# Performance work log

Hardware: AMD Instinct MI355X
Metric: run time of the kernel (lower is better)

The kernel has to match this reference:

```python
import jax, jax.numpy as jnp
import numpy as np

NX, NY = 512, 512
NT = 240
STRIDE = 4
H = 1e-3
DT = 5e-8
F0 = 100000.0
T0 = 6e-6
AMP = 1.0
GAUSS_A = 5e6
RHO = 1600.0
C_INIT = dict(C11=1e11, C22=1e10, C12=8e9, C16=2.5e10, C26=3e9, C66=1.2e10)
C_LO, C_HI = 1e9, 1e13


def setup_inputs() -> dict:
    # Ricker wavelet source signal (full time resolution)
    t = np.arange(NT) * DT
    tau = t - T0
    pf = (np.pi * F0 * tau) ** 2
    signal = (AMP * (1.0 - 2.0 * pf) * np.exp(-pf)).astype(np.float32)
    # Gaussian point-load spatial distribution centered at (0,0)
    Lx, Ly = H * (NX - 1), H * (NY - 1)
    x = np.linspace(-Lx / 2, Lx / 2, NX, dtype=np.float64)
    y = np.linspace(-Ly / 2, Ly / 2, NY, dtype=np.float64)
    X, Y = np.meshgrid(x, y, indexing='ij')
    r2 = X ** 2 + Y ** 2
    gauss = (GAUSS_A / np.pi * np.exp(-GAUSS_A * r2)).astype(np.float32)
    return {
        'log_C11': jnp.array([np.log(C_INIT['C11'])], dtype=jnp.float32),
        'log_C22': jnp.array([np.log(C_INIT['C22'])], dtype=jnp.float32),
        'log_C12': jnp.array([np.log(C_INIT['C12'])], dtype=jnp.float32),
        'log_C16': jnp.array([np.log(C_INIT['C16'])], dtype=jnp.float32),
        'log_C26': jnp.array([np.log(C_INIT['C26'])], dtype=jnp.float32),
        'log_C66': jnp.array([np.log(C_INIT['C66'])], dtype=jnp.float32),
        'rho': jnp.array([RHO], dtype=jnp.float32),
        'source_signal': jnp.asarray(signal),
        'gaussian_dist': jnp.asarray(gauss),
    }


def _stencils(u, h_inv_sq):
    # u: (B, nx, ny), zero-padded 3x3 FD stencils (conv2d_fixed equivalent)
    p = jnp.pad(u, ((0, 0), (1, 1), (1, 1)))
    dxx = (p[:, 2:, 1:-1] + p[:, :-2, 1:-1] - 2.0 * u) * h_inv_sq
    dyy = (p[:, 1:-1, 2:] + p[:, 1:-1, :-2] - 2.0 * u) * h_inv_sq
    dxy = 0.25 * (p[:, :-2, :-2] - p[:, :-2, 2:] - p[:, 2:, :-2] + p[:, 2:, 2:]) * h_inv_sq
    return dxx, dyy, dxy


def _simulate(log_Cs, rho, source_signal, gaussian_dist):
    log_C11, log_C22, log_C12, log_C16, log_C26, log_C66 = log_Cs
    C11 = jnp.clip(jnp.exp(log_C11[0]), C_LO, C_HI)
    C22 = jnp.clip(jnp.exp(log_C22[0]), C_LO, C_HI)
    C12 = jnp.clip(jnp.exp(log_C12[0]), C_LO, C_HI)
    C16 = jnp.clip(jnp.exp(log_C16[0]), C_LO, C_HI)
    C26 = jnp.clip(jnp.exp(log_C26[0]), C_LO, C_HI)
    C66 = jnp.clip(jnp.exp(log_C66[0]), C_LO, C_HI)
    r = rho[0]
    h_inv_sq = jnp.float32(1.0 / (H * H))
    dt2 = jnp.float32(DT * DT)
    g = gaussian_dist[None]  # (1, nx, ny)
    zeros = jnp.zeros((1, NX, NY), dtype=jnp.float32)

    def step(carry, f_amp):
        ux1, uy1, ux2, uy2 = carry
        # source on y component
        force_y = f_amp * g
        dxx_ux, dyy_ux, dxy_ux = _stencils(ux1, h_inv_sq)
        dxx_uy, dyy_uy, dxy_uy = _stencils(uy1, h_inv_sq)
        Lux = (C11 * dxx_ux + C66 * dyy_ux + (C12 + C66) * dxy_uy
               + 2.0 * C16 * dxy_ux + C16 * dxx_uy + C26 * dyy_uy) / r
        Luy = (C66 * dxx_uy + C22 * dyy_uy + (C12 + C66) * dxy_ux
               + C16 * dxx_ux + C26 * dyy_ux + 2.0 * C26 * dxy_uy + force_y) / r
        ux_new = 2.0 * ux1 - ux2 + dt2 * Lux
        uy_new = 2.0 * uy1 - uy2 + dt2 * Luy
        return (ux_new, uy_new, ux1, uy1), (ux_new, uy_new)

    init = (zeros, zeros, zeros, zeros)
    _, (ux_hist, uy_hist) = jax.lax.scan(step, init, source_signal)
    # (nt, 1, nx, ny) -> (1, nt, nx, ny), then PRIMARY time stride subsample
    ux_fields = jnp.moveaxis(ux_hist, 0, 1)[:, ::STRIDE]
    uy_fields = jnp.moveaxis(uy_hist, 0, 1)[:, ::STRIDE]
    return ux_fields, uy_fields


def reference(log_C11, log_C22, log_C12, log_C16, log_C26, log_C66, rho, source_signal, gaussian_dist):
    return _simulate((log_C11, log_C22, log_C12, log_C16, log_C26, log_C66),
                     rho, source_signal, gaussian_dist)
```

## Files before the change

kernel.cpp:

```cpp
#include <hip/hip_runtime.h>

#define NXg    512
#define Sg     262144
#define NFRg   60
#define Kg     8
#define NCHUNK 30
#define Tg     16
#define Eg     32
#define RCg    30
#define CELg   900
#define NTB    1024

__global__ __launch_bounds__(512)
void cfrp_init(float2* __restrict__ ws2)
{
    const int gt = (int)blockIdx.x * 512 + (int)threadIdx.x;
    ws2[gt] = make_float2(0.f, 0.f);
}

__global__ __launch_bounds__(NTB, 8)
void cfrp_chunk(const float* __restrict__ lc11, const float* __restrict__ lc22,
                const float* __restrict__ lc12, const float* __restrict__ lc16,
                const float* __restrict__ lc26, const float* __restrict__ lc66,
                const float* __restrict__ rho_p, const float* __restrict__ sig,
                const float* __restrict__ gauss, float* __restrict__ out,
                const float2* __restrict__ gcur, const float2* __restrict__ gprev,
                float2* __restrict__ ncur, float2* __restrict__ nprev,
                int T0)
{
    __shared__ float2 sf[2][Eg * Eg];

    const int tid = (int)threadIdx.x;
    const int w  = (int)blockIdx.x;
    const int q  = w & 7;
    const int r_ = w >> 3;
    const int ti = q * 4 + (r_ >> 5);
    const int tj = r_ & 31;
    const int oi = ti * Tg - Kg;
    const int oj = tj * Tg - Kg;

    const float C11 = fminf(fmaxf(expf(lc11[0]), 1e9f), 1e13f);
    const float C22 = fminf(fmaxf(expf(lc22[0]), 1e9f), 1e13f);
    const float C12 = fminf(fmaxf(expf(lc12[0]), 1e9f), 1e13f);
    const float C16 = fminf(fmaxf(expf(lc16[0]), 1e9f), 1e13f);
    const float C26 = fminf(fmaxf(expf(lc26[0]), 1e9f), 1e13f);
    const float C66 = fminf(fmaxf(expf(lc66[0]), 1e9f), 1e13f);
    const float r    = rho_p[0];
    const float dt2  = 2.5e-15f;
    const float kk   = dt2 * 1e6f / r;
    const float kc11 = kk * C11, kc22 = kk * C22, kc66 = kk * C66;
    const float kc16 = kk * C16, kc26 = kk * C26;
    const float kc1266 = kk * (C12 + C66);
    const float kc16x2 = 2.0f * kc16;
    const float kc26x2 = 2.0f * kc26;
    const float gsc = dt2 / r;

    {
        const int rr = tid >> 5, cc = tid & 31;
        const int gi = oi + rr, gj = oj + cc;
        const bool inbb = ((unsigned)gi < NXg) && ((unsigned)gj < NXg);
        float2 v = make_float2(0.f, 0.f);
        if (inbb) v = gcur[gi * NXg + gj];
        sf[0][tid] = v;
        sf[1][tid] = v;
    }

    const bool activ = tid < CELg;
    const int  ii = activ ? tid : (CELg - 1);
    const int  rr = ii / RCg + 1;
    const int  cc = ii - (rr - 1) * RCg + 1;
    const int  la = (rr << 5) + cc;
    const int  gi = oi + rr, gj = oj + cc;
    const bool inb = ((unsigned)gi < NXg) && ((unsigned)gj < NXg);
    const int  go = gi * NXg + gj;
    const bool own = activ && rr >= Kg && rr < Kg + Tg
                           && cc >= Kg && cc < Kg + Tg;
    float2 pv = make_float2(0.f, 0.f);
    float  gf = 0.f;
    if (inb) {
        pv = gprev[go];
        gf = gauss[go] * gsc;
    }
    __syncthreads();

    float2 cv = sf[0][la];

    const float2* cur = sf[0];
    float2*       nxt = sf[1];

    #pragma unroll
    for (int st = 0; st < Kg; ++st) {
        const float fa = sig[T0 + st];
        const float2 Nn = cur[la - Eg];
        const float2 Ss = cur[la + Eg];
        const float2 Ww = cur[la - 1];
        const float2 Ee = cur[la + 1];
        const float2 NW = cur[la - Eg - 1];
        const float2 NE = cur[la - Eg + 1];
        const float2 SW = cur[la + Eg - 1];
        const float2 SE = cur[la + Eg + 1];
        const float cx = cv.x, cy = cv.y;

        const float sxx_x = Nn.x + Ss.x - 2.0f * cx;
        const float syy_x = Ww.x + Ee.x - 2.0f * cx;
        const float sxy_x = 0.25f * (NW.x - NE.x - SW.x + SE.x);
        const float sxx_y = Nn.y + Ss.y - 2.0f * cy;
        const float syy_y = Ww.y + Ee.y - 2.0f * cy;
        const float sxy_y = 0.25f * (NW.y - NE.y - SW.y + SE.y);

        const float lux = kc11 * sxx_x + kc66 * syy_x + kc1266 * sxy_y
                        + kc16x2 * sxy_x + kc16 * sxx_y + kc26 * syy_y;
        const float luy = kc66 * sxx_y + kc22 * syy_y + kc1266 * sxy_x
                        + kc16 * sxx_x + kc26 * syy_x + kc26x2 * sxy_y
                        + fa * gf;

        float vx = 2.0f * cx - pv.x + lux;
        float vy = 2.0f * cy - pv.y + luy;
        vx = inb ? vx : 0.0f;
        vy = inb ? vy : 0.0f;
        pv = cv;
        cv = make_float2(vx, vy);

        nxt[la] = cv;

        if ((st & 3) == 0) {
            if (own) {
                const int fo = ((T0 + st) >> 2) * Sg + go;
                out[fo] = vx;
                out[fo + NFRg * Sg] = vy;
            }
        }
        __syncthreads();
        float2* tmp = (float2*)cur; cur = nxt; nxt = tmp;
    }

    if (own) {
        ncur[go]  = cv;
        nprev[go] = pv;
    }
}

extern "C" void kernel_launch(void* const* d_in, const int* in_sizes, int n_in,
                              void* d_out, int out_size, void* d_ws, size_t ws_size,
                              hipStream_t stream) {
    const float* lc11  = (const float*)d_in[0];
    const float* lc22  = (const float*)d_in[1];
    const float* lc12  = (const float*)d_in[2];
    const float* lc16  = (const float*)d_in[3];
    const float* lc26  = (const float*)d_in[4];
    const float* lc66  = (const float*)d_in[5];
    const float* rho_p = (const float*)d_in[6];
    const float* sig   = (const float*)d_in[7];
    const float* gauss = (const float*)d_in[8];
    float* out = (float*)d_out;
    float2* ws2 = (float2*)d_ws;

    float2* Ac = ws2;           float2* Ap = ws2 + Sg;
    float2* Bc = ws2 + 2 * Sg;  float2* Bp = ws2 + 3 * Sg;

    hipLaunchKernelGGL(cfrp_init, dim3(2 * Sg / 512), dim3(512), 0, stream, ws2);

    for (int c = 0; c < NCHUNK; ++c) {
        float2 *rc, *rp, *wc, *wp;
        if (c & 1) { rc = Bc; rp = Bp; wc = Ac; wp = Ap; }
        else       { rc = Ac; rp = Ap; wc = Bc; wp = Bp; }
        hipLaunchKernelGGL(cfrp_chunk, dim3(1024), dim3(NTB), 0, stream,
                           lc11, lc22, lc12, lc16, lc26, lc66, rho_p, sig,
                           gauss, out, rc, rp, wc, wp, c * Kg);
    }
}
```

Baseline: 663.8 us.

## Enlarge temporal-blocking tile to 32x32 with four cells per thread

Grows each block's owned tile from 16x16 to 32x32 (halo extent 48) and runs 256 blocks of 576 threads. Each thread now updates four adjacent cells, loading them with vectorized float4 LDS reads and reusing neighbour values across the four cells. Global loads and stores of state and output frames are also float4-vectorized. The aim is to cut the halo recompute overhead (larger tile to halo ratio) and the LDS traffic per cell, at the cost of fewer blocks (256 on a 256-CU device) and more registers per thread.

```diff
diff --git a/kernel.cpp b/kernel.cpp
--- a/kernel.cpp
+++ b/kernel.cpp
@@ -5,20 +5,20 @@
 #define NFRg   60
 #define Kg     8
 #define NCHUNK 30
-#define Tg     16
-#define Eg     32
-#define RCg    30
-#define CELg   900
-#define NTB    1024
+#define Tg     32
+#define Eg     48
+#define EJP    50
+#define NSEGR  12
+#define NTHR   576
 
 __global__ __launch_bounds__(512)
-void cfrp_init(float2* __restrict__ ws2)
+void cfrp_init(float4* __restrict__ ws4)
 {
     const int gt = (int)blockIdx.x * 512 + (int)threadIdx.x;
-    ws2[gt] = make_float2(0.f, 0.f);
+    ws4[gt] = make_float4(0.f, 0.f, 0.f, 0.f);
 }
 
-__global__ __launch_bounds__(NTB, 8)
+__global__ __launch_bounds__(NTHR)
 void cfrp_chunk(const float* __restrict__ lc11, const float* __restrict__ lc22,
                 const float* __restrict__ lc12, const float* __restrict__ lc16,
                 const float* __restrict__ lc26, const float* __restrict__ lc66,
@@ -26,16 +26,16 @@
                 const float* __restrict__ gauss, float* __restrict__ out,
                 const float2* __restrict__ gcur, const float2* __restrict__ gprev,
                 float2* __restrict__ ncur, float2* __restrict__ nprev,
-                int T0)
+                int TB)
 {
-    __shared__ float2 sf[2][Eg * Eg];
+    __shared__ float2 sf[2][Eg * EJP];
 
     const int tid = (int)threadIdx.x;
     const int w  = (int)blockIdx.x;
     const int q  = w & 7;
     const int r_ = w >> 3;
-    const int ti = q * 4 + (r_ >> 5);
-    const int tj = r_ & 31;
+    const int ti = q * 2 + (r_ >> 4);
+    const int tj = r_ & 15;
     const int oi = ti * Tg - Kg;
     const int oj = tj * Tg - Kg;
 
@@ -45,89 +45,142 @@
     const float C16 = fminf(fmaxf(expf(lc16[0]), 1e9f), 1e13f);
     const float C26 = fminf(fmaxf(expf(lc26[0]), 1e9f), 1e13f);
     const float C66 = fminf(fmaxf(expf(lc66[0]), 1e9f), 1e13f);
-    const float r    = rho_p[0];
+    const float rh   = rho_p[0];
     const float dt2  = 2.5e-15f;
-    const float kk   = dt2 * 1e6f / r;
+    const float kk   = dt2 * 1e6f / rh;
     const float kc11 = kk * C11, kc22 = kk * C22, kc66 = kk * C66;
     const float kc16 = kk * C16, kc26 = kk * C26;
     const float kc1266 = kk * (C12 + C66);
     const float kc16x2 = 2.0f * kc16;
     const float kc26x2 = 2.0f * kc26;
-    const float gsc = dt2 / r;
-
+    const float gsc = dt2 / rh;
+
+    #pragma unroll
+    for (int s = 0; s < 2; ++s) {
+        const int p  = tid + s * NTHR;
+        const int rr = p / 24;
+        const int cp = (p - rr * 24) * 2;
+        const int gi = oi + rr;
+        const int gj = oj + cp;
+        float4 v = make_float4(0.f, 0.f, 0.f, 0.f);
+        if (((unsigned)gi < NXg) && ((unsigned)gj < NXg))
+            v = *(const float4*)&gcur[gi * NXg + gj];
+        const int li = rr * EJP + cp;
+        *(float4*)&sf[0][li] = v;
+        *(float4*)&sf[1][li] = v;
+    }
+    if (tid < Eg) {
+        const int li = tid * EJP + Eg;
+        *(float4*)&sf[0][li] = make_float4(0.f, 0.f, 0.f, 0.f);
+        *(float4*)&sf[1][li] = make_float4(0.f, 0.f, 0.f, 0.f);
+    }
+
+    const int  srow = tid / NSEGR;
+    const int  scol = tid - srow * NSEGR;
+    const bool act  = (srow >= 1) && (srow <= Eg - 2);
+    const int  c0   = scol * 4;
+    const int  gi   = oi + srow;
+    const int  gj0  = oj + c0;
+    const int  idxC = srow * EJP + c0;
+    const bool rin  = (unsigned)gi < NXg;
+    bool inb0 = rin && ((unsigned)(gj0 + 0) < NXg);
+    bool inb1 = rin && ((unsigned)(gj0 + 1) < NXg);
+    bool inb2 = rin && ((unsigned)(gj0 + 2) < NXg);
+    bool inb3 = rin && ((unsigned)(gj0 + 3) < NXg);
+    const bool own = (srow >= Kg) && (srow < Kg + Tg) && (scol >= 2) && (scol <= 9);
+    const int  go0 = gi * NXg + gj0;
+
+    float2 pv0 = {0.f,0.f}, pv1 = {0.f,0.f}, pv2 = {0.f,0.f}, pv3 = {0.f,0.f};
+    float  gf0 = 0.f, gf1 = 0.f, gf2 = 0.f, gf3 = 0.f;
+    if (act && rin) {
+        if ((unsigned)gj0 < NXg) {
+            const float4 t = *(const float4*)&gprev[go0];
+            pv0 = make_float2(t.x, t.y); pv1 = make_float2(t.z, t.w);
+            const float4 g = *(const float4*)&gauss[go0];
+            gf0 = g.x * gsc; gf1 = g.y * gsc; gf2 = g.z * gsc; gf3 = g.w * gsc;
+        }
+        if ((unsigned)(gj0 + 2) < NXg) {
+            const float4 t = *(const float4*)&gprev[go0 + 2];
+            pv2 = make_float2(t.x, t.y); pv3 = make_float2(t.z, t.w);
+        }
+    }
+    __syncthreads();
+
+    float2 cv0, cv1, cv2, cv3;
     {
-        const int rr = tid >> 5, cc = tid & 31;
-        const int gi = oi + rr, gj = oj + cc;
-        const bool inbb = ((unsigned)gi < NXg) && ((unsigned)gj < NXg);
-        float2 v = make_float2(0.f, 0.f);
-        if (inbb) v = gcur[gi * NXg + gj];
-        sf[0][tid] = v;
-        sf[1][tid] = v;
-    }
-
-    const bool activ = tid < CELg;
-    const int  ii = activ ? tid : (CELg - 1);
-    const int  rr = ii / RCg + 1;
-    const int  cc = ii - (rr - 1) * RCg + 1;
-    const int  la = (rr << 5) + cc;
-    const int  gi = oi + rr, gj = oj + cc;
-    const bool inb = ((unsigned)gi < NXg) && ((unsigned)gj < NXg);
-    const int  go = gi * NXg + gj;
-    const bool own = activ && rr >= Kg && rr < Kg + Tg
-                           && cc >= Kg && cc < Kg + Tg;
-    float2 pv = make_float2(0.f, 0.f);
-    float  gf = 0.f;
-    if (inb) {
-        pv = gprev[go];
-        gf = gauss[go] * gsc;
-    }
-    __syncthreads();
-
-    float2 cv = sf[0][la];
+        const float4 a = *(const float4*)&sf[0][idxC];
+        const float4 b = *(const float4*)&sf[0][idxC + 2];
+        cv0 = make_float2(a.x, a.y); cv1 = make_float2(a.z, a.w);
+        cv2 = make_float2(b.x, b.y); cv3 = make_float2(b.z, b.w);
+    }
 
     const float2* cur = sf[0];
     float2*       nxt = sf[1];
 
     #pragma unroll
     for (int st = 0; st < Kg; ++st) {
-        const float fa = sig[T0 + st];
-        const float2 Nn = cur[la - Eg];
-        const float2 Ss = cur[la + Eg];
-        const float2 Ww = cur[la - 1];
-        const float2 Ee = cur[la + 1];
-        const float2 NW = cur[la - Eg - 1];
-        const float2 NE = cur[la - Eg + 1];
-        const float2 SW = cur[la + Eg - 1];
-        const float2 SE = cur[la + Eg + 1];
-        const float cx = cv.x, cy = cv.y;
-
-        const float sxx_x = Nn.x + Ss.x - 2.0f * cx;
-        const float syy_x = Ww.x + Ee.x - 2.0f * cx;
-        const float sxy_x = 0.25f * (NW.x - NE.x - SW.x + SE.x);
-        const float sxx_y = Nn.y + Ss.y - 2.0f * cy;
-        const float syy_y = Ww.y + Ee.y - 2.0f * cy;
-        const float sxy_y = 0.25f * (NW.y - NE.y - SW.y + SE.y);
-
-        const float lux = kc11 * sxx_x + kc66 * syy_x + kc1266 * sxy_y
-                        + kc16x2 * sxy_x + kc16 * sxx_y + kc26 * syy_y;
-        const float luy = kc66 * sxx_y + kc22 * syy_y + kc1266 * sxy_x
-                        + kc16 * sxx_x + kc26 * syy_x + kc26x2 * sxy_y
-                        + fa * gf;
-
-        float vx = 2.0f * cx - pv.x + lux;
-        float vy = 2.0f * cy - pv.y + luy;
-        vx = inb ? vx : 0.0f;
-        vy = inb ? vy : 0.0f;
-        pv = cv;
-        cv = make_float2(vx, vy);
-
-        nxt[la] = cv;
-
-        if ((st & 3) == 0) {
-            if (own) {
-                const int fo = ((T0 + st) >> 2) * Sg + go;
-                out[fo] = vx;
-                out[fo + NFRg * Sg] = vy;
+        const float fa = sig[TB + st];
+        if (act) {
+            const int iT = idxC - EJP;
+            const int iB = idxC + EJP;
+            const float4 t01 = *(const float4*)&cur[iT];
+            const float4 t23 = *(const float4*)&cur[iT + 2];
+            const float2 twv = cur[iT - 1];
+            const float2 tev = cur[iT + 4];
+            const float4 b01 = *(const float4*)&cur[iB];
+            const float4 b23 = *(const float4*)&cur[iB + 2];
+            const float2 bwv = cur[iB - 1];
+            const float2 bev = cur[iB + 4];
+            const float2 wmv = cur[idxC - 1];
+            const float2 emv = cur[idxC + 4];
+
+            const float2 ta0 = twv, ta1 = make_float2(t01.x, t01.y),
+                         ta2 = make_float2(t01.z, t01.w),
+                         ta3 = make_float2(t23.x, t23.y),
+                         ta4 = make_float2(t23.z, t23.w), ta5 = tev;
+            const float2 ba0 = bwv, ba1 = make_float2(b01.x, b01.y),
+                         ba2 = make_float2(b01.z, b01.w),
+                         ba3 = make_float2(b23.x, b23.y),
+                         ba4 = make_float2(b23.z, b23.w), ba5 = bev;
+
+            float2 nv0, nv1, nv2, nv3;
+            #define CELLSTEP(nv, NW, N, NE, Wt, C, Et, SW, S, SE, P, GF, INB)   \
+            {                                                                    \
+                const float sxx_x = N.x + S.x - 2.0f * C.x;                      \
+                const float syy_x = Wt.x + Et.x - 2.0f * C.x;                    \
+                const float sxy_x = 0.25f * (NW.x - NE.x - SW.x + SE.x);         \
+                const float sxx_y = N.y + S.y - 2.0f * C.y;                      \
+                const float syy_y = Wt.y + Et.y - 2.0f * C.y;                    \
+                const float sxy_y = 0.25f * (NW.y - NE.y - SW.y + SE.y);         \
+                const float lux = kc11 * sxx_x + kc66 * syy_x + kc1266 * sxy_y   \
+                                + kc16x2 * sxy_x + kc16 * sxx_y + kc26 * syy_y;  \
+                const float luy = kc66 * sxx_y + kc22 * syy_y + kc1266 * sxy_x   \
+                                + kc16 * sxx_x + kc26 * syy_x + kc26x2 * sxy_y   \
+                                + fa * GF;                                       \
+                float vx = 2.0f * C.x - P.x + lux;                               \
+                float vy = 2.0f * C.y - P.y + luy;                               \
+                vx = INB ? vx : 0.0f;                                            \
+                vy = INB ? vy : 0.0f;                                            \
+                nv = make_float2(vx, vy);                                        \
+            }
+            CELLSTEP(nv0, ta0, ta1, ta2, wmv, cv0, cv1, ba0, ba1, ba2, pv0, gf0, inb0)
+            CELLSTEP(nv1, ta1, ta2, ta3, cv0, cv1, cv2, ba1, ba2, ba3, pv1, gf1, inb1)
+            CELLSTEP(nv2, ta2, ta3, ta4, cv1, cv2, cv3, ba2, ba3, ba4, pv2, gf2, inb2)
+            CELLSTEP(nv3, ta3, ta4, ta5, cv2, cv3, emv, ba3, ba4, ba5, pv3, gf3, inb3)
+            #undef CELLSTEP
+
+            pv0 = cv0; pv1 = cv1; pv2 = cv2; pv3 = cv3;
+            cv0 = nv0; cv1 = nv1; cv2 = nv2; cv3 = nv3;
+
+            *(float4*)&nxt[idxC]     = make_float4(cv0.x, cv0.y, cv1.x, cv1.y);
+            *(float4*)&nxt[idxC + 2] = make_float4(cv2.x, cv2.y, cv3.x, cv3.y);
+
+            if (((st & 3) == 0) && own) {
+                const int fr = (TB + st) >> 2;
+                *(float4*)&out[fr * Sg + go0] =
+                    make_float4(cv0.x, cv1.x, cv2.x, cv3.x);
+                *(float4*)&out[(fr + NFRg) * Sg + go0] =
+                    make_float4(cv0.y, cv1.y, cv2.y, cv3.y);
             }
         }
         __syncthreads();
@@ -135,8 +188,10 @@
     }
 
     if (own) {
-        ncur[go]  = cv;
-        nprev[go] = pv;
+        *(float4*)&ncur[go0]      = make_float4(cv0.x, cv0.y, cv1.x, cv1.y);
+        *(float4*)&ncur[go0 + 2]  = make_float4(cv2.x, cv2.y, cv3.x, cv3.y);
+        *(float4*)&nprev[go0]     = make_float4(pv0.x, pv0.y, pv1.x, pv1.y);
+        *(float4*)&nprev[go0 + 2] = make_float4(pv2.x, pv2.y, pv3.x, pv3.y);
     }
 }
 
@@ -152,19 +207,19 @@
     const float* rho_p = (const float*)d_in[6];
     const float* sig   = (const float*)d_in[7];
     const float* gauss = (const float*)d_in[8];
-    float* out = (float*)d_out;
+    float* out  = (float*)d_out;
     float2* ws2 = (float2*)d_ws;
 
     float2* Ac = ws2;           float2* Ap = ws2 + Sg;
     float2* Bc = ws2 + 2 * Sg;  float2* Bp = ws2 + 3 * Sg;
 
-    hipLaunchKernelGGL(cfrp_init, dim3(2 * Sg / 512), dim3(512), 0, stream, ws2);
+    hipLaunchKernelGGL(cfrp_init, dim3(512), dim3(512), 0, stream, (float4*)d_ws);
 
     for (int c = 0; c < NCHUNK; ++c) {
         float2 *rc, *rp, *wc, *wp;
         if (c & 1) { rc = Bc; rp = Bp; wc = Ac; wp = Ap; }
         else       { rc = Ac; rp = Ap; wc = Bc; wp = Bp; }
-        hipLaunchKernelGGL(cfrp_chunk, dim3(1024), dim3(NTB), 0, stream,
+        hipLaunchKernelGGL(cfrp_chunk, dim3(256), dim3(NTHR), 0, stream,
                            lc11, lc22, lc12, lc16, lc26, lc66, rho_p, sig,
                            gauss, out, rc, rp, wc, wp, c * Kg);
     }
```

Result: faster. 548.0 us (-17.4%).
